# Kernel tuning notes

Measured on AMD Instinct MI355X. Metric: run time of the kernel, lower is better.

Reference implementation:

```python
import jax, jax.numpy as jnp
import numpy as np

N, B, E, H, L, NF = 32768, 2048, 524288, 128, 7, 10
NODE_F = 60  # 10 frames * (loc 3 + vel 3)
OUT_F = 30   # 10 frames * 3


def _mlp(x, W1, b1, W2, b2):
    return jax.nn.relu(x @ W1 + b1) @ W2 + b2


def _lin(key, fan_in, fan_out):
    s = 1.0 / np.sqrt(fan_in)
    kw, kb = jax.random.split(key)
    W = jax.random.uniform(kw, (fan_in, fan_out), jnp.float32, -s, s)
    b = jax.random.uniform(kb, (fan_out,), jnp.float32, -s, s)
    return W, b


def setup_inputs() -> dict:
    key = jax.random.key(0)
    ks = jax.random.split(key, 12)
    p = {}
    p["loc"] = jax.random.normal(ks[0], (N, NF, 3), jnp.float32)
    p["vel"] = jax.random.normal(ks[1], (N, NF, 3), jnp.float32)
    p["y"] = jax.random.normal(ks[2], (N, NF, 3), jnp.float32)
    p["edge_index"] = jax.random.randint(ks[3], (2, E), 0, N, dtype=jnp.int64)
    p["batch_size"] = B
    # embedder: Linear(60,H) -> ReLU -> Linear(H,H)
    p["emb_W1"], p["emb_b1"] = _lin(ks[4], NODE_F, H)
    p["emb_W2"], p["emb_b2"] = _lin(ks[5], H, H)
    # per-layer message net Linear(2H,H)->ReLU->Linear(H,H); update net Linear(2H,H)->ReLU->Linear(H,H)
    mW1, mb1, mW2, mb2, uW1, ub1, uW2, ub2 = [], [], [], [], [], [], [], []
    for i in range(L):
        k = jax.random.fold_in(ks[6], i)
        k1, k2, k3, k4 = jax.random.split(k, 4)
        a, b = _lin(k1, 2 * H, H); mW1.append(a); mb1.append(b)
        a, b = _lin(k2, H, H); mW2.append(a); mb2.append(b)
        a, b = _lin(k3, 2 * H, H); uW1.append(a); ub1.append(b)
        a, b = _lin(k4, H, H); uW2.append(a); ub2.append(b)
    p["msg_W1"] = jnp.stack(mW1); p["msg_b1"] = jnp.stack(mb1)
    p["msg_W2"] = jnp.stack(mW2); p["msg_b2"] = jnp.stack(mb2)
    p["upd_W1"] = jnp.stack(uW1); p["upd_b1"] = jnp.stack(ub1)
    p["upd_W2"] = jnp.stack(uW2); p["upd_b2"] = jnp.stack(ub2)
    # head: Linear(H,H) -> ReLU -> Linear(H,30)
    p["head_W1"], p["head_b1"] = _lin(ks[7], H, H)
    p["head_W2"], p["head_b2"] = _lin(ks[8], H, OUT_F)
    return p


def reference(loc, vel, y, edge_index, batch_size,
              emb_W1, emb_b1, emb_W2, emb_b2,
              msg_W1, msg_b1, msg_W2, msg_b2,
              upd_W1, upd_b1, upd_W2, upd_b2,
              head_W1, head_b1, head_W2, head_b2):
    n = loc.shape[0]
    src, dst = edge_index[0], edge_index[1]  # x_j = x[src], x_i = x[dst] (PyG source_to_target)
    x = jnp.concatenate([loc, vel], axis=-1).reshape(n, -1)  # (N, 60)
    x = _mlp(x, emb_W1, emb_b1, emb_W2, emb_b2)              # (N, H)
    for i in range(L):
        m_in = jnp.concatenate([x[dst], x[src]], axis=-1)    # (E, 2H) cat(x_i, x_j)
        msg = _mlp(m_in, msg_W1[i], msg_b1[i], msg_W2[i], msg_b2[i])  # (E, H)
        agg = jax.ops.segment_sum(msg, dst, num_segments=n)  # scatter-add at targets
        x = _mlp(jnp.concatenate([x, agg], axis=-1), upd_W1[i], upd_b1[i], upd_W2[i], upd_b2[i])
    x = _mlp(x, head_W1, head_b1, head_W2, head_b2)          # (N, 30)
    loc_pred = x.reshape(n, NF, 3) + loc
    d = jnp.sqrt(jnp.sum((loc_pred - y) ** 2, axis=-1))      # (N, NF)
    ade_loss = d.reshape(batch_size, -1, NF).mean(axis=-1).mean(axis=-1)  # (B,)
    fde = jnp.sqrt(jnp.sum((loc_pred[:, -1, :] - y[:, -1, :]) ** 2, axis=-1))  # (N,)
    fde_loss = fde.reshape(batch_size, -1).mean(axis=-1)     # (B,)
    backprop_loss = ade_loss.mean()
    return backprop_loss, ade_loss, fde_loss
```

## Files before the change

### kernel.cpp

```cpp
#include <hip/hip_runtime.h>
#include <hip/hip_bf16.h>
#include <stdint.h>

#define HH 128

typedef __attribute__((ext_vector_type(8))) short short8;
typedef __attribute__((ext_vector_type(4))) float floatx4;

typedef __attribute__((address_space(3))) uint32_t lds_u32_t;
typedef const __attribute__((address_space(1))) uint32_t gbl_u32_t;

__device__ __forceinline__ void gl_lds16(const void* g, void* l) {
  __builtin_amdgcn_global_load_lds((gbl_u32_t*)g, (lds_u32_t*)l, 16, 0, 0);
}

__device__ __forceinline__ float bf2f(short v) {
  union { uint32_t u; float f; } x; x.u = ((uint32_t)(uint16_t)v) << 16; return x.f;
}
__device__ __forceinline__ short f2bf(float f) {
  union { float f; uint32_t u; } x; x.f = f;
  uint32_t r = x.u + 0x7fffu + ((x.u >> 16) & 1u);
  return (short)(r >> 16);
}
__device__ __forceinline__ float rdf(const void* p, int i, int fl) {
  return fl ? bf2f(((const short*)p)[i]) : ((const float*)p)[i];
}


__global__ void detect_zero(const int* __restrict__ eidx, int* iflag, int* dflag,
                            int* __restrict__ counts, float* accp,
                            const uint32_t* __restrict__ loc, int N) {
  int g = blockIdx.x * 256 + threadIdx.x;
  if (g < N) counts[g] = 0;
  if (blockIdx.x == 0) {
    __shared__ int nz, cnt;
    if (threadIdx.x == 0) { nz = 0; cnt = 0; *accp = 0.f; }
    __syncthreads();
    int any = 0;
    for (int i = threadIdx.x; i < 1024; i += 256) any |= (eidx[2 * i + 1] != 0);
    if (any) atomicOr(&nz, 1);
    uint32_t u = loc[threadIdx.x];
    int e = (u >> 7) & 0xFF;
    if (e >= 100 && e <= 140) atomicAdd(&cnt, 1);
    __syncthreads();
    if (threadIdx.x == 0) {
      *iflag = (nz == 0) ? 1 : 0;
      *dflag = (cnt >= 192) ? 1 : 0;
    }
  }
}


__global__ void pad_input(const void* __restrict__ loc, const void* __restrict__ vel,
                          short* __restrict__ dst, const int* __restrict__ dflag) {
  int fl = *dflag;
  int idx = blockIdx.x * 256 + threadIdx.x;
  int j = idx & 63, i = idx >> 6;
  short v = 0;
  if (j < 60) {
    int f = j / 6, c = j % 6;
    float x = (c < 3) ? rdf(loc, (i * 10 + f) * 3 + c, fl)
                      : rdf(vel, (i * 10 + f) * 3 + (c - 3), fl);
    v = f2bf(x);
  }
  dst[idx] = v;
}

struct WPrep {
  const void* src[8];
  unsigned long long dstoff[8];
  int L[8], K[8], Nn[8], Kp[8], Np[8];
  int bstart[9];
};

__global__ void prep_w(WPrep a, short* __restrict__ wbase, const int* __restrict__ dflag) {
  int fl = *dflag;
  int b = blockIdx.x;
  int s = 0;
  while (b >= a.bstart[s + 1]) ++s;
  int idx = (b - a.bstart[s]) * 256 + threadIdx.x;
  int Kp = a.Kp[s], Np = a.Np[s], K = a.K[s], Nn = a.Nn[s];
  int tot = a.L[s] * Np * Kp;
  if (idx >= tot) return;
  int k = idx % Kp; int rest = idx / Kp; int n = rest % Np; int l = rest / Np;
  short v = 0;
  if (k < K && n < Nn) v = f2bf(rdf(a.src[s], (l * K + k) * Nn + n, fl));
  wbase[a.dstoff[s] + idx] = v;
}

struct BPrep {
  const void* src[8];
  int n[8];
  int estart[9];
};

__global__ void prep_b(BPrep a, float* __restrict__ bias, const int* __restrict__ dflag) {
  int fl = *dflag;
  int idx = blockIdx.x * 256 + threadIdx.x;
  if (idx >= a.estart[8]) return;
  int s = 0;
  while (idx >= a.estart[s + 1]) ++s;
  int j = idx - a.estart[s];
  bias[idx] = (j < a.n[s]) ? rdf(a.src[s], j, fl) : 0.0f;
}


__global__ void fold_kernel(const short* __restrict__ updW1T, const short* __restrict__ msgW2T,
                            short* __restrict__ updW1Tf, const float* __restrict__ msgB2f,
                            float* __restrict__ b2U) {
  if (blockIdx.x < 896) {
    int idx = blockIdx.x * 256 + threadIdx.x;
    int k = idx & 255; int n = (idx >> 8) & 127; int l = idx >> 15;
    if (k < 128) { updW1Tf[idx] = updW1T[idx]; return; }
    int kk = k - 128;
    const short* w2 = msgW2T + l * 128 * 128;
    const short* u1 = updW1T + l * 128 * 256 + n * 256 + 128;
    float s = 0.f;
    for (int j = 0; j < 128; ++j) s += bf2f(w2[j * 128 + kk]) * bf2f(u1[j]);
    updW1Tf[idx] = f2bf(s);
  } else {
    int idx = (blockIdx.x - 896) * 256 + threadIdx.x;
    if (idx >= 7 * 128) return;
    int n = idx & 127, l = idx >> 7;
    const short* u1 = updW1T + l * 128 * 256 + n * 256 + 128;
    const float* b2 = msgB2f + l * 128;
    float s = 0.f;
    for (int j = 0; j < 128; ++j) s += b2[j] * bf2f(u1[j]);
    b2U[idx] = s;
  }
}


__global__ void hist_kernel(const int* __restrict__ eidx, const int* __restrict__ iflag,
                            int* __restrict__ counts, int E) {
  int e = blockIdx.x * 256 + threadIdx.x;
  if (e >= E) return;
  int fl = *iflag;
  int d = fl ? eidx[2 * (E + e)] : eidx[E + e];
  atomicAdd(&counts[d], 1);
}

__global__ void scan_bsum(const int* __restrict__ counts, int* __restrict__ bsums, int N) {
  int i = blockIdx.x * 256 + threadIdx.x;
  int v = (i < N) ? counts[i] : 0;
#pragma unroll
  for (int off = 1; off < 64; off <<= 1) v += __shfl_xor(v, off);
  __shared__ int ws4[4];
  if ((threadIdx.x & 63) == 0) ws4[threadIdx.x >> 6] = v;
  __syncthreads();
  if (threadIdx.x == 0) bsums[blockIdx.x] = ws4[0] + ws4[1] + ws4[2] + ws4[3];
}

__global__ void scan_final(const int* __restrict__ counts, const int* __restrict__ bsums,
                           int* __restrict__ row_start, int* __restrict__ cursor,
                           float* __restrict__ deg, int N, int E) {
  int t = threadIdx.x;
  __shared__ int shb[2];
  __shared__ int wsum[4];
  int v = (t < 128 && t < (int)blockIdx.x) ? bsums[t] : 0;
#pragma unroll
  for (int off = 1; off < 64; off <<= 1) v += __shfl_xor(v, off);
  if (t == 0) shb[0] = v;
  if (t == 64) shb[1] = v;
  int i = blockIdx.x * 256 + t;
  int c = (i < N) ? counts[i] : 0;
  int lane = t & 63, w = t >> 6;
  int x = c;
#pragma unroll
  for (int off = 1; off < 64; off <<= 1) {
    int u = __shfl_up(x, off);
    if (lane >= off) x += u;
  }
  if (lane == 63) wsum[w] = x;
  __syncthreads();
  int wpre = 0;
#pragma unroll
  for (int k = 0; k < 4; ++k)
    if (k < w) wpre += wsum[k];
  int excl = shb[0] + shb[1] + wpre + x - c;
  if (i < N) {
    row_start[i] = excl;
    cursor[i] = excl;
    deg[i] = (float)c;
  }
  if (i == N - 1) row_start[N] = E;
}

__global__ void scatter_kernel(const int* __restrict__ eidx, const int* __restrict__ iflag,
                               int* __restrict__ cursor, int* __restrict__ ssrc, int E) {
  int e = blockIdx.x * 256 + threadIdx.x;
  if (e >= E) return;
  int fl = *iflag;
  int d = fl ? eidx[2 * (E + e)] : eidx[E + e];
  int sv = fl ? eidx[2 * e] : eidx[e];
  int pos = atomicAdd(&cursor[d], 1);
  ssrc[pos] = sv;
}


__global__ __launch_bounds__(256)
void edge_agg(const float* __restrict__ P, const uint32_t* __restrict__ Qp,
              const int* __restrict__ ssrc, const int* __restrict__ row_start,
              uint32_t* __restrict__ Hagg, int Ntot) {
  int w = threadIdx.x >> 6, lane = threadIdx.x & 63;
  int d = blockIdx.x * 4 + w;
  if (d >= Ntot) return;
  float px = P[(size_t)d * HH + 2 * lane];
  float py = P[(size_t)d * HH + 2 * lane + 1];
  int s0 = row_start[d], s1 = row_start[d + 1];
  float ax = 0.f, ay = 0.f;
  int e = s0;
  for (; e + 4 <= s1; e += 4) {
    int i0 = ssrc[e], i1 = ssrc[e + 1], i2 = ssrc[e + 2], i3 = ssrc[e + 3];
    uint32_t q0 = Qp[(size_t)i0 * 64 + lane];
    uint32_t q1 = Qp[(size_t)i1 * 64 + lane];
    uint32_t q2 = Qp[(size_t)i2 * 64 + lane];
    uint32_t q3 = Qp[(size_t)i3 * 64 + lane];
    float hx, hy;
    hx = px + bf2f((short)(q0 & 0xffff)); hy = py + bf2f((short)(q0 >> 16));
    ax += hx > 0.f ? hx : 0.f; ay += hy > 0.f ? hy : 0.f;
    hx = px + bf2f((short)(q1 & 0xffff)); hy = py + bf2f((short)(q1 >> 16));
    ax += hx > 0.f ? hx : 0.f; ay += hy > 0.f ? hy : 0.f;
    hx = px + bf2f((short)(q2 & 0xffff)); hy = py + bf2f((short)(q2 >> 16));
    ax += hx > 0.f ? hx : 0.f; ay += hy > 0.f ? hy : 0.f;
    hx = px + bf2f((short)(q3 & 0xffff)); hy = py + bf2f((short)(q3 >> 16));
    ax += hx > 0.f ? hx : 0.f; ay += hy > 0.f ? hy : 0.f;
  }
  for (; e < s1; ++e) {
    int i0 = ssrc[e];
    uint32_t q0 = Qp[(size_t)i0 * 64 + lane];
    float hx = px + bf2f((short)(q0 & 0xffff));
    float hy = py + bf2f((short)(q0 >> 16));
    ax += hx > 0.f ? hx : 0.f;
    ay += hy > 0.f ? hy : 0.f;
  }
  uint32_t packed = (uint32_t)(uint16_t)f2bf(ax) | ((uint32_t)(uint16_t)f2bf(ay) << 16);
  Hagg[(size_t)d * 64 + lane] = packed;
}


__device__ __forceinline__ void write_aslots(char* lds, const floatx4 v2[2][8],
                                             int w, int quad, int l16) {
  const int mtgb = w * 2;
#pragma unroll
  for (int mt = 0; mt < 2; ++mt)
#pragma unroll
    for (int nt = 0; nt < 8; ++nt) {
      floatx4 v = v2[mt][nt];
      int s2 = nt >> 1;
      int lpb = 16 * ((nt & 1) * 2 + (l16 >> 3));
      int joff = 2 * (l16 & 7);
      char* base = lds + (size_t)(s2 * 8 + mtgb + mt) * 1024 + joff;
#pragma unroll
      for (int r = 0; r < 4; ++r)
        *(short*)(base + (quad * 4 + r + lpb) * 16) = f2bf(v[r]);
    }
}

template <int NT>
__device__ __forceinline__ void gemm_lds(const char* lds, int mtgb, floatx4 acc[2][NT], int lane) {
#pragma unroll
  for (int s2 = 0; s2 < 4; ++s2) {
    short8 af[2];
#pragma unroll
    for (int mt = 0; mt < 2; ++mt)
      af[mt] = *(const short8*)(lds + (s2 * 8 + mtgb + mt) * 1024 + lane * 16);
    short8 bfr[NT];
#pragma unroll
    for (int t = 0; t < NT; ++t)
      bfr[t] = *(const short8*)(lds + 32768 + (s2 * NT + t) * 1024 + lane * 16);
#pragma unroll
    for (int mt = 0; mt < 2; ++mt)
#pragma unroll
      for (int t = 0; t < NT; ++t)
        acc[mt][t] = __builtin_amdgcn_mfma_f32_16x16x32_bf16(af[mt], bfr[t], acc[mt][t], 0, 0, 0);
  }
}


template <int MODE>
__global__ __launch_bounds__(256, 2)
void mlp_fused(const short* __restrict__ Asrc, const short* __restrict__ Asrc2,
               const short* __restrict__ W1T, const float* __restrict__ b1,
               const short* __restrict__ W2T, const float* __restrict__ b2,
               const float* __restrict__ deg, const float* __restrict__ b2Uv,
               const short* __restrict__ pqW1, const float* __restrict__ pqB1,
               const short* __restrict__ pq2W, const float* __restrict__ pq2B,
               short* __restrict__ xout, float* __restrict__ Pout,
               short* __restrict__ Qout, float* __restrict__ out32) {
  constexpr int K1 = (MODE == 0) ? 64 : 256;
  constexpr int NS = K1 / 32;
  constexpr int PQS = (MODE == 3) ? 128 : 256;

  __shared__ __align__(16) char lds[65536];

  const int tid = threadIdx.x;
  const int w = tid >> 6, lane = tid & 63;
  const int quad = lane >> 4, l16 = lane & 15;
  const int R0 = blockIdx.x * 128;
  const int mtgb = w * 2;

#pragma unroll
  for (int c = 0; c < NS * 2; ++c) {
    int slot = w * (NS * 2) + c;
    int s = slot >> 3, t = slot & 7;
    int n = t * 16 + l16, k = s * 32 + quad * 8;
    gl_lds16(W1T + n * K1 + k, lds + slot * 1024 + lane * 16);
  }

  short8 afrag[NS][2];
  if constexpr (MODE == 0) {
#pragma unroll
    for (int mt = 0; mt < 2; ++mt) {
      int m = R0 + w * 32 + mt * 16 + l16;
      const short* pr = Asrc + (size_t)m * 64;
#pragma unroll
      for (int s = 0; s < NS; ++s) afrag[s][mt] = *(const short8*)(pr + s * 32 + quad * 8);
    }
  } else {
#pragma unroll
    for (int mt = 0; mt < 2; ++mt) {
      int m = R0 + w * 32 + mt * 16 + l16;
      const short* pr = Asrc + (size_t)m * HH;
      const short* ar = Asrc2 + (size_t)m * HH;
#pragma unroll
      for (int s = 0; s < 4; ++s) {
        afrag[s][mt] = *(const short8*)(pr + s * 32 + quad * 8);
        afrag[s + 4][mt] = *(const short8*)(ar + s * 32 + quad * 8);
      }
    }
  }

  float b1f[8], b2f[8], pb1[8], b2u[8];
  float dvals[2][4];
#pragma unroll
  for (int t = 0; t < 8; ++t) b1f[t] = b1[t * 16 + l16];
#pragma unroll
  for (int t = 0; t < 8; ++t) b2f[t] = b2[t * 16 + l16];
#pragma unroll
  for (int t = 0; t < 8; ++t) pb1[t] = pqB1[t * 16 + l16];
  if constexpr (MODE != 0) {
#pragma unroll
    for (int t = 0; t < 8; ++t) b2u[t] = b2Uv[t * 16 + l16];
#pragma unroll
    for (int mt = 0; mt < 2; ++mt)
#pragma unroll
      for (int r = 0; r < 4; ++r)
        dvals[mt][r] = deg[R0 + w * 32 + mt * 16 + quad * 4 + r];
  }

  __syncthreads();

  floatx4 zero4 = {0.f, 0.f, 0.f, 0.f};
  floatx4 acc[2][8];
#pragma unroll
  for (int mt = 0; mt < 2; ++mt)
#pragma unroll
    for (int t = 0; t < 8; ++t) acc[mt][t] = zero4;
#pragma unroll
  for (int s = 0; s < NS; ++s) {
    short8 bfrag[8];
#pragma unroll
    for (int t = 0; t < 8; ++t)
      bfrag[t] = *(const short8*)(lds + (s * 8 + t) * 1024 + lane * 16);
#pragma unroll
    for (int mt = 0; mt < 2; ++mt)
#pragma unroll
      for (int t = 0; t < 8; ++t)
        acc[mt][t] = __builtin_amdgcn_mfma_f32_16x16x32_bf16(afrag[s][mt], bfrag[t], acc[mt][t], 0, 0, 0);
  }

  __syncthreads();

#pragma unroll
  for (int c = 0; c < 8; ++c) {
    int slot = w * 8 + c;
    int n = c * 16 + l16, k = w * 32 + quad * 8;
    gl_lds16(W2T + n * HH + k, lds + 32768 + slot * 1024 + lane * 16);
  }
  {
    floatx4 hv[2][8];
#pragma unroll
    for (int mt = 0; mt < 2; ++mt)
#pragma unroll
      for (int nt = 0; nt < 8; ++nt)
#pragma unroll
        for (int r = 0; r < 4; ++r) {
          float h = acc[mt][nt][r] + b1f[nt];
          if constexpr (MODE != 0) h += dvals[mt][r] * b2u[nt];
          hv[mt][nt][r] = h > 0.f ? h : 0.f;
        }
    write_aslots(lds, hv, w, quad, l16);
  }

  __syncthreads();

  floatx4 acc2[2][8];
#pragma unroll
  for (int mt = 0; mt < 2; ++mt)
#pragma unroll
    for (int t = 0; t < 8; ++t) acc2[mt][t] = zero4;
  gemm_lds<8>(lds, mtgb, acc2, lane);

  floatx4 xv[2][8];
#pragma unroll
  for (int mt = 0; mt < 2; ++mt)
#pragma unroll
    for (int nt = 0; nt < 8; ++nt)
#pragma unroll
      for (int r = 0; r < 4; ++r)
        xv[mt][nt][r] = acc2[mt][nt][r] + b2f[nt];

  if constexpr (MODE != 3) {
#pragma unroll
    for (int mt = 0; mt < 2; ++mt)
#pragma unroll
      for (int nt = 0; nt < 8; ++nt) {
        int col = nt * 16 + l16;
#pragma unroll
        for (int r = 0; r < 4; ++r) {
          int row = R0 + w * 32 + mt * 16 + quad * 4 + r;
          xout[(size_t)row * HH + col] = f2bf(xv[mt][nt][r]);
        }
      }
  }

  __syncthreads();

  write_aslots(lds, xv, w, quad, l16);
#pragma unroll
  for (int c = 0; c < 8; ++c) {
    int slot = w * 8 + c;
    int n = c * 16 + l16, k = w * 32 + quad * 8;
    gl_lds16(pqW1 + n * PQS + k, lds + 32768 + slot * 1024 + lane * 16);
  }

  __syncthreads();

  floatx4 accc[2][8];
#pragma unroll
  for (int mt = 0; mt < 2; ++mt)
#pragma unroll
    for (int t = 0; t < 8; ++t) accc[mt][t] = zero4;
  gemm_lds<8>(lds, mtgb, accc, lane);

  if constexpr (MODE == 3) {
    floatx4 h2[2][8];
#pragma unroll
    for (int mt = 0; mt < 2; ++mt)
#pragma unroll
      for (int nt = 0; nt < 8; ++nt)
#pragma unroll
        for (int r = 0; r < 4; ++r) {
          float h = accc[mt][nt][r] + pb1[nt];
          h2[mt][nt][r] = h > 0.f ? h : 0.f;
        }
    __syncthreads();
    write_aslots(lds, h2, w, quad, l16);
#pragma unroll
    for (int c = 0; c < 2; ++c) {
      int slot = w * 2 + c;
      int n = c * 16 + l16, k = w * 32 + quad * 8;
      gl_lds16(pq2W + n * 128 + k, lds + 32768 + slot * 1024 + lane * 16);
    }
    __syncthreads();
    floatx4 acco[2][2];
#pragma unroll
    for (int mt = 0; mt < 2; ++mt)
#pragma unroll
      for (int t = 0; t < 2; ++t) acco[mt][t] = zero4;
    gemm_lds<2>(lds, mtgb, acco, lane);
    float ob[2];
#pragma unroll
    for (int t = 0; t < 2; ++t) ob[t] = pq2B[t * 16 + l16];
#pragma unroll
    for (int mt = 0; mt < 2; ++mt)
#pragma unroll
      for (int nt = 0; nt < 2; ++nt) {
        int col = nt * 16 + l16;
#pragma unroll
        for (int r = 0; r < 4; ++r) {
          int row = R0 + w * 32 + mt * 16 + quad * 4 + r;
          out32[(size_t)row * 32 + col] = acco[mt][nt][r] + ob[nt];
        }
      }
  } else {
#pragma unroll
    for (int mt = 0; mt < 2; ++mt)
#pragma unroll
      for (int nt = 0; nt < 8; ++nt) {
        int col = nt * 16 + l16;
#pragma unroll
        for (int r = 0; r < 4; ++r) {
          int row = R0 + w * 32 + mt * 16 + quad * 4 + r;
          Pout[(size_t)row * HH + col] = accc[mt][nt][r] + pb1[nt];
        }
      }
    __syncthreads();
#pragma unroll
    for (int c = 0; c < 8; ++c) {
      int slot = w * 8 + c;
      int n = c * 16 + l16, k = w * 32 + quad * 8;
      gl_lds16(pqW1 + n * 256 + 128 + k, lds + 32768 + slot * 1024 + lane * 16);
    }
    __syncthreads();
    floatx4 accq[2][8];
#pragma unroll
    for (int mt = 0; mt < 2; ++mt)
#pragma unroll
      for (int t = 0; t < 8; ++t) accq[mt][t] = zero4;
    gemm_lds<8>(lds, mtgb, accq, lane);
#pragma unroll
    for (int mt = 0; mt < 2; ++mt)
#pragma unroll
      for (int nt = 0; nt < 8; ++nt) {
        int col = nt * 16 + l16;
#pragma unroll
        for (int r = 0; r < 4; ++r) {
          int row = R0 + w * 32 + mt * 16 + quad * 4 + r;
          Qout[(size_t)row * HH + col] = f2bf(accq[mt][nt][r]);
        }
      }
  }
}


__global__ void loss_kernel(const float* __restrict__ out32, const void* __restrict__ loc,
                            const void* __restrict__ yv, const int* __restrict__ dflag,
                            float* __restrict__ out, float* __restrict__ acc, int NB) {
  int fl = *dflag;
  int i = blockIdx.x * 256 + threadIdx.x;
  const float* o = out32 + (size_t)i * 32;
  float dsum = 0.f, fde = 0.f;
#pragma unroll
  for (int f = 0; f < 10; ++f) {
    float dx = o[f * 3 + 0] + rdf(loc, i * 30 + f * 3 + 0, fl) - rdf(yv, i * 30 + f * 3 + 0, fl);
    float dy = o[f * 3 + 1] + rdf(loc, i * 30 + f * 3 + 1, fl) - rdf(yv, i * 30 + f * 3 + 1, fl);
    float dz = o[f * 3 + 2] + rdf(loc, i * 30 + f * 3 + 2, fl) - rdf(yv, i * 30 + f * 3 + 2, fl);
    float d = sqrtf(dx * dx + dy * dy + dz * dz);
    dsum += d;
    if (f == 9) fde = d;
  }
#pragma unroll
  for (int m = 1; m < 16; m <<= 1) {
    dsum += __shfl_xor(dsum, m);
    fde += __shfl_xor(fde, m);
  }
  if ((threadIdx.x & 15) == 0) {
    int b = i >> 4;
    out[1 + b] = dsum / 160.0f;
    out[1 + NB + b] = fde / 16.0f;
    unsafeAtomicAdd(acc, dsum);
  }
}

__global__ void final_kernel(const float* __restrict__ acc, float* __restrict__ out, float inv) {
  if (threadIdx.x == 0) out[0] = *acc * inv;
}


extern "C" void kernel_launch(void* const* d_in, const int* in_sizes, int n_in,
                              void* d_out, int out_size, void* d_ws, size_t ws_size,
                              hipStream_t stream) {
  const void* loc = d_in[0];
  const void* vel = d_in[1];
  const void* yv = d_in[2];
  const int* eidx = (const int*)d_in[3];

  const int N = in_sizes[0] / 30;
  const int E = in_sizes[3] / 2;
  const int L = 7;
  const int NB = N / 16;

  const size_t MB = 1024 * 1024;
  char* ws = (char*)d_ws;
  short* x = (short*)ws;
  float* P = (float*)(ws + 8 * MB);
  short* Qs = (short*)(ws + 24 * MB);
  short* Hagg = (short*)(ws + 32 * MB);
  short* updW1Tf = (short*)(ws + 40 * MB);
  int* bsums = (int*)(ws + 41 * MB);
  short* wbase = (short*)(ws + 48 * MB);
  const unsigned long long OFF_EMBW1 = 0;
  const unsigned long long OFF_EMBW2 = 8192;
  const unsigned long long OFF_HEADW1 = 24576;
  const unsigned long long OFF_HEADW2 = 40960;
  const unsigned long long OFF_MSGW1 = 45056;
  const unsigned long long OFF_MSGW2 = 274432;
  const unsigned long long OFF_UPDW1 = 389120;
  const unsigned long long OFF_UPDW2 = 618496;
  short* embW1T = wbase + OFF_EMBW1;
  short* embW2T = wbase + OFF_EMBW2;
  short* headW1T = wbase + OFF_HEADW1;
  short* headW2T = wbase + OFF_HEADW2;
  short* msgW1T = wbase + OFF_MSGW1;
  short* msgW2T = wbase + OFF_MSGW2;
  short* updW1T = wbase + OFF_UPDW1;
  short* updW2T = wbase + OFF_UPDW2;
  float* bias = (float*)(ws + 49 * MB + 512 * 1024);
  float* embB1f = bias;
  float* embB2f = bias + 128;
  float* msgB1f = bias + 256;
  float* msgB2f = bias + 1152;
  float* updB1f = bias + 2048;
  float* updB2f = bias + 2944;
  float* headB1f = bias + 3840;
  float* headB2f = bias + 3968;
  float* b2U = bias + 4096;
  int* counts = (int*)(ws + 49 * MB + 768 * 1024);
  int* row_start = (int*)(ws + 50 * MB);
  int* cursor = (int*)(ws + 50 * MB + 256 * 1024);
  float* deg = (float*)(ws + 50 * MB + 512 * 1024);
  int* iflag = (int*)(ws + 50 * MB + 768 * 1024);
  int* dflag = iflag + 16;
  float* accp = (float*)(iflag + 32);
  int* ssrc = (int*)(ws + 51 * MB);
  short* in64 = (short*)(ws + 53 * MB);
  float* out32 = (float*)(ws + 57 * MB);

  const int NBLK = (N + 255) / 256;

  detect_zero<<<NBLK, 256, 0, stream>>>(eidx, iflag, dflag, counts, accp,
                                        (const uint32_t*)loc, N);
  hist_kernel<<<(E + 255) / 256, 256, 0, stream>>>(eidx, iflag, counts, E);
  scan_bsum<<<NBLK, 256, 0, stream>>>(counts, bsums, N);
  scan_final<<<NBLK, 256, 0, stream>>>(counts, bsums, row_start, cursor, deg, N, E);
  scatter_kernel<<<(E + 255) / 256, 256, 0, stream>>>(eidx, iflag, cursor, ssrc, E);

  pad_input<<<(N * 64) / 256, 256, 0, stream>>>(loc, vel, in64, dflag);

  {
    WPrep a;
    const void* srcs[8] = {d_in[5], d_in[7], d_in[17], d_in[19],
                           d_in[9], d_in[11], d_in[13], d_in[15]};
    unsigned long long offs[8] = {OFF_EMBW1, OFF_EMBW2, OFF_HEADW1, OFF_HEADW2,
                                  OFF_MSGW1, OFF_MSGW2, OFF_UPDW1, OFF_UPDW2};
    int Ls[8] = {1, 1, 1, 1, 7, 7, 7, 7};
    int Ks[8] = {60, 128, 128, 128, 256, 128, 256, 128};
    int Ns[8] = {128, 128, 128, 30, 128, 128, 128, 128};
    int Kps[8] = {64, 128, 128, 128, 256, 128, 256, 128};
    int Nps[8] = {128, 128, 128, 32, 128, 128, 128, 128};
    int cum = 0;
    for (int s = 0; s < 8; ++s) {
      a.src[s] = srcs[s]; a.dstoff[s] = offs[s];
      a.L[s] = Ls[s]; a.K[s] = Ks[s]; a.Nn[s] = Ns[s]; a.Kp[s] = Kps[s]; a.Np[s] = Nps[s];
      a.bstart[s] = cum;
      cum += (Ls[s] * Nps[s] * Kps[s] + 255) / 256;
    }
    a.bstart[8] = cum;
    prep_w<<<cum, 256, 0, stream>>>(a, wbase, dflag);
  }
  {
    BPrep a;
    const void* srcs[8] = {d_in[6], d_in[8], d_in[10], d_in[12],
                           d_in[14], d_in[16], d_in[18], d_in[20]};
    int ns[8] = {128, 128, 896, 896, 896, 896, 128, 30};
    int es[9] = {0, 128, 256, 1152, 2048, 2944, 3840, 3968, 4000};
    for (int s = 0; s < 8; ++s) { a.src[s] = srcs[s]; a.n[s] = ns[s]; a.estart[s] = es[s]; }
    a.estart[8] = es[8];
    prep_b<<<16, 256, 0, stream>>>(a, bias, dflag);
  }

  fold_kernel<<<900, 256, 0, stream>>>(updW1T, msgW2T, updW1Tf, msgB2f, b2U);

  mlp_fused<0><<<N / 128, 256, 0, stream>>>(in64, nullptr,
      embW1T, embB1f, embW2T, embB2f, nullptr, nullptr,
      msgW1T, msgB1f, nullptr, nullptr, x, P, Qs, nullptr);

  for (int l = 0; l < L; ++l) {
    edge_agg<<<(N + 3) / 4, 256, 0, stream>>>(P, (const uint32_t*)Qs, ssrc, row_start,
                                              (uint32_t*)Hagg, N);
    if (l < L - 1) {
      mlp_fused<2><<<N / 128, 256, 0, stream>>>(x, Hagg,
          updW1Tf + l * 128 * 256, updB1f + l * 128, updW2T + l * 128 * 128, updB2f + l * 128,
          deg, b2U + l * 128,
          msgW1T + (l + 1) * 128 * 256, msgB1f + (l + 1) * 128, nullptr, nullptr,
          x, P, Qs, nullptr);
    } else {
      mlp_fused<3><<<N / 128, 256, 0, stream>>>(x, Hagg,
          updW1Tf + l * 128 * 256, updB1f + l * 128, updW2T + l * 128 * 128, updB2f + l * 128,
          deg, b2U + l * 128,
          headW1T, headB1f, headW2T, headB2f,
          nullptr, nullptr, nullptr, out32);
    }
  }

  loss_kernel<<<N / 256, 256, 0, stream>>>(out32, loc, yv, dflag, (float*)d_out, accp, NB);
  final_kernel<<<1, 64, 0, stream>>>(accp, (float*)d_out, 1.0f / 327680.0f);
}
```

Measured before the change: 533.0 us.

## Split MLP tile across 8 waves, store P in bf16, unroll edge gather by 8

The fused MLP kernel now runs with 512 threads, arranged as 8 waves in a 4x2 grid over rows and column halves. Each wave computes only 64 output columns, which halves its accumulator registers and should raise latency hiding. The P projection is stored as bf16 instead of fp32, halving its write and read traffic in the edge aggregation. The edge gather loop is unrolled to 8 independent loads to get more memory-level parallelism. Storing P in bf16 adds rounding to the message pre-activation.

```diff
diff --git a/kernel.cpp b/kernel.cpp
--- a/kernel.cpp
+++ b/kernel.cpp
@@ -199,32 +199,32 @@
 
 
 __global__ __launch_bounds__(256)
-void edge_agg(const float* __restrict__ P, const uint32_t* __restrict__ Qp,
+void edge_agg(const uint32_t* __restrict__ Pp, const uint32_t* __restrict__ Qp,
               const int* __restrict__ ssrc, const int* __restrict__ row_start,
               uint32_t* __restrict__ Hagg, int Ntot) {
   int w = threadIdx.x >> 6, lane = threadIdx.x & 63;
   int d = blockIdx.x * 4 + w;
   if (d >= Ntot) return;
-  float px = P[(size_t)d * HH + 2 * lane];
-  float py = P[(size_t)d * HH + 2 * lane + 1];
+  uint32_t pv = Pp[(size_t)d * 64 + lane];
+  float px = bf2f((short)(pv & 0xffff));
+  float py = bf2f((short)(pv >> 16));
   int s0 = row_start[d], s1 = row_start[d + 1];
   float ax = 0.f, ay = 0.f;
   int e = s0;
-  for (; e + 4 <= s1; e += 4) {
-    int i0 = ssrc[e], i1 = ssrc[e + 1], i2 = ssrc[e + 2], i3 = ssrc[e + 3];
-    uint32_t q0 = Qp[(size_t)i0 * 64 + lane];
-    uint32_t q1 = Qp[(size_t)i1 * 64 + lane];
-    uint32_t q2 = Qp[(size_t)i2 * 64 + lane];
-    uint32_t q3 = Qp[(size_t)i3 * 64 + lane];
-    float hx, hy;
-    hx = px + bf2f((short)(q0 & 0xffff)); hy = py + bf2f((short)(q0 >> 16));
-    ax += hx > 0.f ? hx : 0.f; ay += hy > 0.f ? hy : 0.f;
-    hx = px + bf2f((short)(q1 & 0xffff)); hy = py + bf2f((short)(q1 >> 16));
-    ax += hx > 0.f ? hx : 0.f; ay += hy > 0.f ? hy : 0.f;
-    hx = px + bf2f((short)(q2 & 0xffff)); hy = py + bf2f((short)(q2 >> 16));
-    ax += hx > 0.f ? hx : 0.f; ay += hy > 0.f ? hy : 0.f;
-    hx = px + bf2f((short)(q3 & 0xffff)); hy = py + bf2f((short)(q3 >> 16));
-    ax += hx > 0.f ? hx : 0.f; ay += hy > 0.f ? hy : 0.f;
+  for (; e + 8 <= s1; e += 8) {
+    int idx[8];
+    uint32_t q[8];
+#pragma unroll
+    for (int u = 0; u < 8; ++u) idx[u] = ssrc[e + u];
+#pragma unroll
+    for (int u = 0; u < 8; ++u) q[u] = Qp[(size_t)idx[u] * 64 + lane];
+#pragma unroll
+    for (int u = 0; u < 8; ++u) {
+      float hx = px + bf2f((short)(q[u] & 0xffff));
+      float hy = py + bf2f((short)(q[u] >> 16));
+      ax += hx > 0.f ? hx : 0.f;
+      ay += hy > 0.f ? hy : 0.f;
+    }
   }
   for (; e < s1; ++e) {
     int i0 = ssrc[e];
@@ -239,54 +239,54 @@
 }
 
 
-__device__ __forceinline__ void write_aslots(char* lds, const floatx4 v2[2][8],
-                                             int w, int quad, int l16) {
-  const int mtgb = w * 2;
-#pragma unroll
-  for (int mt = 0; mt < 2; ++mt)
-#pragma unroll
-    for (int nt = 0; nt < 8; ++nt) {
-      floatx4 v = v2[mt][nt];
-      int s2 = nt >> 1;
-      int lpb = 16 * ((nt & 1) * 2 + (l16 >> 3));
-      int joff = 2 * (l16 & 7);
-      char* base = lds + (size_t)(s2 * 8 + mtgb + mt) * 1024 + joff;
+__device__ __forceinline__ void write_aslots_q(char* lds, const floatx4 v[2][4],
+                                               int wr, int wc, int quad, int l16) {
+#pragma unroll
+  for (int mt = 0; mt < 2; ++mt) {
+    int g = wr * 2 + mt;
+#pragma unroll
+    for (int nt = 0; nt < 4; ++nt) {
+      int s2 = wc * 2 + (nt >> 1);
+      int qc = (nt & 1) * 2 + (l16 >> 3);
+      char* base = lds + (size_t)(s2 * 8 + g) * 1024 + 2 * (l16 & 7);
 #pragma unroll
       for (int r = 0; r < 4; ++r)
-        *(short*)(base + (quad * 4 + r + lpb) * 16) = f2bf(v[r]);
-    }
-}
-
-template <int NT>
-__device__ __forceinline__ void gemm_lds(const char* lds, int mtgb, floatx4 acc[2][NT], int lane) {
+        *(short*)(base + (quad * 4 + r + 16 * qc) * 16) = f2bf(v[mt][nt][r]);
+    }
+  }
+}
+
+template <int NT, int TS>
+__device__ __forceinline__ void gemm_q(const char* lds, int wr, int wc,
+                                       floatx4 acc[2][NT], int lane) {
 #pragma unroll
   for (int s2 = 0; s2 < 4; ++s2) {
     short8 af[2];
 #pragma unroll
     for (int mt = 0; mt < 2; ++mt)
-      af[mt] = *(const short8*)(lds + (s2 * 8 + mtgb + mt) * 1024 + lane * 16);
-    short8 bfr[NT];
-#pragma unroll
-    for (int t = 0; t < NT; ++t)
-      bfr[t] = *(const short8*)(lds + 32768 + (s2 * NT + t) * 1024 + lane * 16);
-#pragma unroll
-    for (int mt = 0; mt < 2; ++mt)
-#pragma unroll
-      for (int t = 0; t < NT; ++t)
-        acc[mt][t] = __builtin_amdgcn_mfma_f32_16x16x32_bf16(af[mt], bfr[t], acc[mt][t], 0, 0, 0);
+      af[mt] = *(const short8*)(lds + (s2 * 8 + wr * 2 + mt) * 1024 + lane * 16);
+    short8 bf[NT];
+#pragma unroll
+    for (int nt = 0; nt < NT; ++nt)
+      bf[nt] = *(const short8*)(lds + 32768 + (s2 * TS + wc * NT + nt) * 1024 + lane * 16);
+#pragma unroll
+    for (int mt = 0; mt < 2; ++mt)
+#pragma unroll
+      for (int nt = 0; nt < NT; ++nt)
+        acc[mt][nt] = __builtin_amdgcn_mfma_f32_16x16x32_bf16(af[mt], bf[nt], acc[mt][nt], 0, 0, 0);
   }
 }
 
 
 template <int MODE>
-__global__ __launch_bounds__(256, 2)
+__global__ __launch_bounds__(512, 2)
 void mlp_fused(const short* __restrict__ Asrc, const short* __restrict__ Asrc2,
                const short* __restrict__ W1T, const float* __restrict__ b1,
                const short* __restrict__ W2T, const float* __restrict__ b2,
                const float* __restrict__ deg, const float* __restrict__ b2Uv,
                const short* __restrict__ pqW1, const float* __restrict__ pqB1,
                const short* __restrict__ pq2W, const float* __restrict__ pq2B,
-               short* __restrict__ xout, float* __restrict__ Pout,
+               short* __restrict__ xout, short* __restrict__ Pout,
                short* __restrict__ Qout, float* __restrict__ out32) {
   constexpr int K1 = (MODE == 0) ? 64 : 256;
   constexpr int NS = K1 / 32;
@@ -297,12 +297,13 @@
   const int tid = threadIdx.x;
   const int w = tid >> 6, lane = tid & 63;
   const int quad = lane >> 4, l16 = lane & 15;
+  const int wr = w >> 1, wc = w & 1;
   const int R0 = blockIdx.x * 128;
-  const int mtgb = w * 2;
-
-#pragma unroll
-  for (int c = 0; c < NS * 2; ++c) {
-    int slot = w * (NS * 2) + c;
+  const int CB = wc * 64;
+
+#pragma unroll
+  for (int c = 0; c < NS; ++c) {
+    int slot = w * NS + c;
     int s = slot >> 3, t = slot & 7;
     int n = t * 16 + l16, k = s * 32 + quad * 8;
     gl_lds16(W1T + n * K1 + k, lds + slot * 1024 + lane * 16);
@@ -312,7 +313,7 @@
   if constexpr (MODE == 0) {
 #pragma unroll
     for (int mt = 0; mt < 2; ++mt) {
-      int m = R0 + w * 32 + mt * 16 + l16;
+      int m = R0 + wr * 32 + mt * 16 + l16;
       const short* pr = Asrc + (size_t)m * 64;
 #pragma unroll
       for (int s = 0; s < NS; ++s) afrag[s][mt] = *(const short8*)(pr + s * 32 + quad * 8);
@@ -320,7 +321,7 @@
   } else {
 #pragma unroll
     for (int mt = 0; mt < 2; ++mt) {
-      int m = R0 + w * 32 + mt * 16 + l16;
+      int m = R0 + wr * 32 + mt * 16 + l16;
       const short* pr = Asrc + (size_t)m * HH;
       const short* ar = Asrc2 + (size_t)m * HH;
 #pragma unroll
@@ -331,82 +332,84 @@
     }
   }
 
-  float b1f[8], b2f[8], pb1[8], b2u[8];
+  float b1f[4], b2f[4], pb1[4], b2u[4];
   float dvals[2][4];
 #pragma unroll
-  for (int t = 0; t < 8; ++t) b1f[t] = b1[t * 16 + l16];
-#pragma unroll
-  for (int t = 0; t < 8; ++t) b2f[t] = b2[t * 16 + l16];
-#pragma unroll
-  for (int t = 0; t < 8; ++t) pb1[t] = pqB1[t * 16 + l16];
+  for (int t = 0; t < 4; ++t) {
+    int col = CB + t * 16 + l16;
+    b1f[t] = b1[col];
+    b2f[t] = b2[col];
+    pb1[t] = pqB1[col];
+  }
   if constexpr (MODE != 0) {
 #pragma unroll
-    for (int t = 0; t < 8; ++t) b2u[t] = b2Uv[t * 16 + l16];
+    for (int t = 0; t < 4; ++t) b2u[t] = b2Uv[CB + t * 16 + l16];
 #pragma unroll
     for (int mt = 0; mt < 2; ++mt)
 #pragma unroll
       for (int r = 0; r < 4; ++r)
-        dvals[mt][r] = deg[R0 + w * 32 + mt * 16 + quad * 4 + r];
+        dvals[mt][r] = deg[R0 + wr * 32 + mt * 16 + quad * 4 + r];
   }
 
   __syncthreads();
 
   floatx4 zero4 = {0.f, 0.f, 0.f, 0.f};
-  floatx4 acc[2][8];
+  floatx4 acc[2][4];
 #pragma unroll
   for (int mt = 0; mt < 2; ++mt)
 #pragma unroll
-    for (int t = 0; t < 8; ++t) acc[mt][t] = zero4;
+    for (int t = 0; t < 4; ++t) acc[mt][t] = zero4;
 #pragma unroll
   for (int s = 0; s < NS; ++s) {
-    short8 bfrag[8];
-#pragma unroll
-    for (int t = 0; t < 8; ++t)
-      bfrag[t] = *(const short8*)(lds + (s * 8 + t) * 1024 + lane * 16);
-#pragma unroll
-    for (int mt = 0; mt < 2; ++mt)
-#pragma unroll
-      for (int t = 0; t < 8; ++t)
-        acc[mt][t] = __builtin_amdgcn_mfma_f32_16x16x32_bf16(afrag[s][mt], bfrag[t], acc[mt][t], 0, 0, 0);
+    short8 bfrag[4];
+#pragma unroll
+    for (int nt = 0; nt < 4; ++nt)
+      bfrag[nt] = *(const short8*)(lds + (s * 8 + wc * 4 + nt) * 1024 + lane * 16);
+#pragma unroll
+    for (int mt = 0; mt < 2; ++mt)
+#pragma unroll
+      for (int nt = 0; nt < 4; ++nt)
+        acc[mt][nt] = __builtin_amdgcn_mfma_f32_16x16x32_bf16(afrag[s][mt], bfrag[nt], acc[mt][nt], 0, 0, 0);
   }
 
   __syncthreads();
 
 #pragma unroll
-  for (int c = 0; c < 8; ++c) {
-    int slot = w * 8 + c;
-    int n = c * 16 + l16, k = w * 32 + quad * 8;
+  for (int c = 0; c < 4; ++c) {
+    int slot = w * 4 + c;
+    int s2 = slot >> 3, t = slot & 7;
+    int n = t * 16 + l16, k = s2 * 32 + quad * 8;
     gl_lds16(W2T + n * HH + k, lds + 32768 + slot * 1024 + lane * 16);
   }
   {
-    floatx4 hv[2][8];
-#pragma unroll
-    for (int mt = 0; mt < 2; ++mt)
-#pragma unroll
-      for (int nt = 0; nt < 8; ++nt)
+    floatx4 hv[2][4];
+#pragma unroll
+    for (int mt = 0; mt < 2; ++mt)
+#pragma unroll
+      for (int nt = 0; nt < 4; ++nt)
 #pragma unroll
         for (int r = 0; r < 4; ++r) {
           float h = acc[mt][nt][r] + b1f[nt];
           if constexpr (MODE != 0) h += dvals[mt][r] * b2u[nt];
           hv[mt][nt][r] = h > 0.f ? h : 0.f;
         }
-    write_aslots(lds, hv, w, quad, l16);
+    write_aslots_q(lds, hv, wr, wc, quad, l16);
   }
 
   __syncthreads();
 
-  floatx4 acc2[2][8];
+  floatx4 acc2[2][4];
 #pragma unroll
   for (int mt = 0; mt < 2; ++mt)
 #pragma unroll
-    for (int t = 0; t < 8; ++t) acc2[mt][t] = zero4;
-  gemm_lds<8>(lds, mtgb, acc2, lane);
-
-  floatx4 xv[2][8];
+    for (int t = 0; t < 4; ++t) acc2[mt][t] = zero4;
+  gemm_q<4, 8>(lds, wr, wc, acc2, lane);
+
+  floatx4 xv[2][4];
 #pragma unroll
   for (int mt = 0; mt < 2; ++mt)
 #pragma unroll
-    for (int nt = 0; nt < 8; ++nt)
+    for (int nt = 0; nt < 4; ++nt)
 #pragma unroll
       for (int r = 0; r < 4; ++r)
         xv[mt][nt][r] = acc2[mt][nt][r] + b2f[nt];
@@ -415,11 +418,11 @@
 #pragma unroll
     for (int mt = 0; mt < 2; ++mt)
 #pragma unroll
-      for (int nt = 0; nt < 8; ++nt) {
-        int col = nt * 16 + l16;
+      for (int nt = 0; nt < 4; ++nt) {
+        int col = CB + nt * 16 + l16;
 #pragma unroll
         for (int r = 0; r < 4; ++r) {
-          int row = R0 + w * 32 + mt * 16 + quad * 4 + r;
+          int row = R0 + wr * 32 + mt * 16 + quad * 4 + r;
           xout[(size_t)row * HH + col] = f2bf(xv[mt][nt][r]);
         }
       }
@@ -427,97 +430,92 @@
 
   __syncthreads();
 
-  write_aslots(lds, xv, w, quad, l16);
-#pragma unroll
-  for (int c = 0; c < 8; ++c) {
-    int slot = w * 8 + c;
-    int n = c * 16 + l16, k = w * 32 + quad * 8;
+  write_aslots_q(lds, xv, wr, wc, quad, l16);
+#pragma unroll
+  for (int c = 0; c < 4; ++c) {
+    int slot = w * 4 + c;
+    int s2 = slot >> 3, t = slot & 7;
+    int n = t * 16 + l16, k = s2 * 32 + quad * 8;
     gl_lds16(pqW1 + n * PQS + k, lds + 32768 + slot * 1024 + lane * 16);
   }
 
   __syncthreads();
 
-  floatx4 accc[2][8];
+  floatx4 accc[2][4];
 #pragma unroll
   for (int mt = 0; mt < 2; ++mt)
 #pragma unroll
-    for (int t = 0; t < 8; ++t) accc[mt][t] = zero4;
-  gemm_lds<8>(lds, mtgb, accc, lane);
+    for (int t = 0; t < 4; ++t) accc[mt][t] = zero4;
+  gemm_q<4, 8>(lds, wr, wc, accc, lane);
 
   if constexpr (MODE == 3) {
-    floatx4 h2[2][8];
-#pragma unroll
-    for (int mt = 0; mt < 2; ++mt)
-#pragma unroll
-      for (int nt = 0; nt < 8; ++nt)
+    floatx4 h2[2][4];
+#pragma unroll
+    for (int mt = 0; mt < 2; ++mt)
+#pragma unroll
+      for (int nt = 0; nt < 4; ++nt)
 #pragma unroll
         for (int r = 0; r < 4; ++r) {
           float h = accc[mt][nt][r] + pb1[nt];
           h2[mt][nt][r] = h > 0.f ? h : 0.f;
         }
     __syncthreads();
-    write_aslots(lds, h2, w, quad, l16);
-#pragma unroll
-    for (int c = 0; c < 2; ++c) {
-      int slot = w * 2 + c;
-      int n = c * 16 + l16, k = w * 32 + quad * 8;
-      gl_lds16(pq2W + n * 128 + k, lds + 32768 + slot * 1024 + lane * 16);
+    write_aslots_q(lds, h2, wr, wc, quad, l16);
+    {
+      int s2 = w >> 1, t = w & 1;
+      int n = t * 16 + l16, k = s2 * 32 + quad * 8;
+      gl_lds16(pq2W + n * 128 + k, lds + 32768 + w * 1024 + lane * 16);
     }
     __syncthreads();
-    floatx4 acco[2][2];
-#pragma unroll
-    for (int mt = 0; mt < 2; ++mt)
-#pragma unroll
-      for (int t = 0; t < 2; ++t) acco[mt][t] = zero4;
-    gemm_lds<2>(lds, mtgb, acco, lane);
-    float ob[2];
-#pragma unroll
-    for (int t = 0; t < 2; ++t) ob[t] = pq2B[t * 16 + l16];
-#pragma unroll
-    for (int mt = 0; mt < 2; ++mt)
-#pragma unroll
-      for (int nt = 0; nt < 2; ++nt) {
-        int col = nt * 16 + l16;
+    floatx4 acco[2][1];
+#pragma unroll
+    for (int mt = 0; mt < 2; ++mt) acco[mt][0] = zero4;
+    gemm_q<1, 2>(lds, wr, wc, acco, lane);
+    float ob = pq2B[wc * 16 + l16];
+#pragma unroll
+    for (int mt = 0; mt < 2; ++mt) {
+      int col = wc * 16 + l16;
+#pragma unroll
+      for (int r = 0; r < 4; ++r) {
+        int row = R0 + wr * 32 + mt * 16 + quad * 4 + r;
+        out32[(size_t)row * 32 + col] = acco[mt][0][r] + ob;
+      }
+    }
+  } else {
+#pragma unroll
+    for (int mt = 0; mt < 2; ++mt)
+#pragma unroll
+      for (int nt = 0; nt < 4; ++nt) {
+        int col = CB + nt * 16 + l16;
 #pragma unroll
         for (int r = 0; r < 4; ++r) {
-          int row = R0 + w * 32 + mt * 16 + quad * 4 + r;
-          out32[(size_t)row * 32 + col] = acco[mt][nt][r] + ob[nt];
-        }
-      }
-  } else {
-#pragma unroll
-    for (int mt = 0; mt < 2; ++mt)
-#pragma unroll
-      for (int nt = 0; nt < 8; ++nt) {
-        int col = nt * 16 + l16;
-#pragma unroll
-        for (int r = 0; r < 4; ++r) {
-          int row = R0 + w * 32 + mt * 16 + quad * 4 + r;
-          Pout[(size_t)row * HH + col] = accc[mt][nt][r] + pb1[nt];
+          int row = R0 + wr * 32 + mt * 16 + quad * 4 + r;
+          Pout[(size_t)row * HH + col] = f2bf(accc[mt][nt][r] + pb1[nt]);
         }
       }
     __syncthreads();
 #pragma unroll
-    for (int c = 0; c < 8; ++c) {
-      int slot = w * 8 + c;
-      int n = c * 16 + l16, k = w * 32 + quad * 8;
+    for (int c = 0; c < 4; ++c) {
+      int slot = w * 4 + c;
+      int s2 = slot >> 3, t = slot & 7;
+      int n = t * 16 + l16, k = s2 * 32 + quad * 8;
       gl_lds16(pqW1 + n * 256 + 128 + k, lds + 32768 + slot * 1024 + lane * 16);
     }
     __syncthreads();
-    floatx4 accq[2][8];
-#pragma unroll
-    for (int mt = 0; mt < 2; ++mt)
-#pragma unroll
-      for (int t = 0; t < 8; ++t) accq[mt][t] = zero4;
-    gemm_lds<8>(lds, mtgb, accq, lane);
-#pragma unroll
-    for (int mt = 0; mt < 2; ++mt)
-#pragma unroll
-      for (int nt = 0; nt < 8; ++nt) {
-        int col = nt * 16 + l16;
+    floatx4 accq[2][4];
+#pragma unroll
+    for (int mt = 0; mt < 2; ++mt)
+#pragma unroll
+      for (int t = 0; t < 4; ++t) accq[mt][t] = zero4;
+    gemm_q<4, 8>(lds, wr, wc, accq, lane);
+#pragma unroll
+    for (int mt = 0; mt < 2; ++mt)
+#pragma unroll
+      for (int nt = 0; nt < 4; ++nt) {
+        int col = CB + nt * 16 + l16;
 #pragma unroll
         for (int r = 0; r < 4; ++r) {
-          int row = R0 + w * 32 + mt * 16 + quad * 4 + r;
+          int row = R0 + wr * 32 + mt * 16 + quad * 4 + r;
           Qout[(size_t)row * HH + col] = f2bf(accq[mt][nt][r]);
         }
       }
@@ -575,7 +573,7 @@
   const size_t MB = 1024 * 1024;
   char* ws = (char*)d_ws;
   short* x = (short*)ws;
-  float* P = (float*)(ws + 8 * MB);
+  short* P = (short*)(ws + 8 * MB);
   short* Qs = (short*)(ws + 24 * MB);
   short* Hagg = (short*)(ws + 32 * MB);
   short* updW1Tf = (short*)(ws + 40 * MB);
@@ -663,21 +661,21 @@
 
   fold_kernel<<<900, 256, 0, stream>>>(updW1T, msgW2T, updW1Tf, msgB2f, b2U);
 
-  mlp_fused<0><<<N / 128, 256, 0, stream>>>(in64, nullptr,
+  mlp_fused<0><<<N / 128, 512, 0, stream>>>(in64, nullptr,
       embW1T, embB1f, embW2T, embB2f, nullptr, nullptr,
       msgW1T, msgB1f, nullptr, nullptr, x, P, Qs, nullptr);
 
   for (int l = 0; l < L; ++l) {
-    edge_agg<<<(N + 3) / 4, 256, 0, stream>>>(P, (const uint32_t*)Qs, ssrc, row_start,
-                                              (uint32_t*)Hagg, N);
+    edge_agg<<<(N + 3) / 4, 256, 0, stream>>>((const uint32_t*)P, (const uint32_t*)Qs,
+                                              ssrc, row_start, (uint32_t*)Hagg, N);
     if (l < L - 1) {
-      mlp_fused<2><<<N / 128, 256, 0, stream>>>(x, Hagg,
+      mlp_fused<2><<<N / 128, 512, 0, stream>>>(x, Hagg,
           updW1Tf + l * 128 * 256, updB1f + l * 128, updW2T + l * 128 * 128, updB2f + l * 128,
           deg, b2U + l * 128,
           msgW1T + (l + 1) * 128 * 256, msgB1f + (l + 1) * 128, nullptr, nullptr,
           x, P, Qs, nullptr);
     } else {
-      mlp_fused<3><<<N / 128, 256, 0, stream>>>(x, Hagg,
+      mlp_fused<3><<<N / 128, 512, 0, stream>>>(x, Hagg,
           updW1Tf + l * 128 * 256, updB1f + l * 128, updW2T + l * 128 * 128, updB2f + l * 128,
           deg, b2U + l * 128,
           headW1T, headB1f, headW2T, headB2f,
```

Result: no change. 531.4 us (-0.3%).
